# Optimization experiments

Measured on AMD Instinct MI355X. Metric: run time of the kernel, lower is better.

Reference implementation:

```python
import jax, jax.numpy as jnp
import numpy as np

B, NC, CARD, NCONT, DIM, DEPTH, HEADS, DH = 4096, 32, 100, 64, 64, 8, 8, 16
DEPTH = 6
INNER = HEADS * DH            # 128
TOTAL_TOKENS = NC * CARD + 2  # 3202 (2 special tokens)
CAT_FLAT = NC * DIM           # 2048
BETA = 0.2


def setup_inputs() -> dict:
    key = jax.random.key(0)
    ks = iter(jax.random.split(key, 32))
    n = lambda shape, s=0.05: jax.random.normal(next(ks), shape, dtype=jnp.float32) * s
    return {
        "x_categ": jax.random.randint(next(ks), (B, NC), 0, CARD),
        "x_cont": jax.random.normal(next(ks), (B, NCONT), dtype=jnp.float32),
        "embed": n((TOTAL_TOKENS, DIM)),
        "ln1_g": jnp.ones((DEPTH, DIM)), "ln1_b": jnp.zeros((DEPTH, DIM)),
        "wqkv": n((DEPTH, DIM, 3 * INNER)),
        "wo": n((DEPTH, INNER, DIM)), "bo": jnp.zeros((DEPTH, DIM)),
        "ln2_g": jnp.ones((DEPTH, DIM)), "ln2_b": jnp.zeros((DEPTH, DIM)),
        "wff1": n((DEPTH, DIM, 8 * DIM)), "bff1": jnp.zeros((DEPTH, 8 * DIM)),
        "wff2": n((DEPTH, 4 * DIM, DIM)), "bff2": jnp.zeros((DEPTH, DIM)),
        "bn_g": jnp.ones((NCONT,)), "bn_b": jnp.zeros((NCONT,)),
        "g0_w": n((CAT_FLAT + NCONT, CAT_FLAT)), "g0_b": jnp.zeros((CAT_FLAT,)),
        "h0_w": n((NCONT, CAT_FLAT)),
        "y1_w": n((CAT_FLAT, NCONT)), "y1_b": jnp.zeros((NCONT,)),
        "g1_w": n((2 * NCONT, NCONT)), "g1_b": jnp.zeros((NCONT,)),
        "h1_w": n((NCONT, NCONT)),
        "fc_w": n((CAT_FLAT + NCONT, 1)), "fc_b": jnp.zeros((1,)),
    }


def _ln(x, g, b):
    mu = x.mean(-1, keepdims=True)
    v = ((x - mu) ** 2).mean(-1, keepdims=True)
    return (x - mu) * jax.lax.rsqrt(v + 1e-5) * g + b


def _split_heads(t):  # [B, N, INNER] -> [B, H, N, DH]
    return t.reshape(B, NC, HEADS, DH).transpose(0, 2, 1, 3)


def _gate_combine(x, y, gw, gb, hw):
    # per-row gated aggregation with norm-scaled residual (DAG_combiner pair)
    g = jax.nn.relu(jnp.concatenate([x, y], axis=-1) @ gw + gb)
    H = g * (y @ hw)
    norm = jnp.linalg.norm(x, axis=1) / (jnp.linalg.norm(H, axis=1) + 1e-12)
    alpha = jnp.clip(norm * BETA, 0.0, 1.0)
    return x + alpha[:, None] * H


def reference(x_categ, x_cont, embed, ln1_g, ln1_b, wqkv, wo, bo, ln2_g, ln2_b,
              wff1, bff1, wff2, bff2, bn_g, bn_b, g0_w, g0_b, h0_w,
              y1_w, y1_b, g1_w, g1_b, h1_w, fc_w, fc_b):
    offsets = 2 + CARD * jnp.arange(NC)          # categories_offset
    tok = x_categ + offsets
    x = embed[tok]                                # [B, NC, DIM]
    scale = DH ** -0.5
    for d in range(DEPTH):
        h = _ln(x, ln1_g[d], ln1_b[d])
        q, k, v = jnp.split(h @ wqkv[d], 3, axis=-1)
        q, k, v = _split_heads(q), _split_heads(k), _split_heads(v)
        sim = jnp.einsum('bhid,bhjd->bhij', q, k) * scale
        attn = jax.nn.softmax(sim, axis=-1)
        o = jnp.einsum('bhij,bhjd->bhid', attn, v)
        o = o.transpose(0, 2, 1, 3).reshape(B, NC, INNER)
        x = x + (o @ wo[d] + bo[d])
        h = _ln(x, ln2_g[d], ln2_b[d])
        f = h @ wff1[d] + bff1[d]
        a, gg = jnp.split(f, 2, axis=-1)
        x = (a * jax.nn.gelu(gg, approximate=False)) @ wff2[d] + bff2[d] + x
    flat_categ = x.reshape(B, CAT_FLAT)
    # BatchNorm1d (train-mode batch stats, biased variance)
    mu = x_cont.mean(0)
    var = ((x_cont - mu) ** 2).mean(0)
    normed = (x_cont - mu) * jax.lax.rsqrt(var + 1e-5) * bn_g + bn_b
    # DAG combiner, dims = [2048, 64]
    c0 = _gate_combine(flat_categ, normed, g0_w, g0_b, h0_w)          # y_dim 64 <= 2048: no y proj
    y1 = flat_categ @ y1_w + y1_b                                      # y_dim 2048 > 64: MLP2 == single Linear
    c1 = _gate_combine(normed, y1, g1_w, g1_b, h1_w)
    logits = jnp.concatenate([c0, c1], axis=-1) @ fc_w + fc_b
    return jax.nn.sigmoid(logits)
```

## Files before the change

### kernel.cpp

```cpp
#include <hip/hip_runtime.h>
#include <hip/hip_bf16.h>

#define B_    4096
#define NC    32
#define DIM   64
#define INNER 128
#define HEADS 8
#define DH    16
#define DEPTH 6
#define NCONT 64
#define CATF  2048
#define KTOT  2112
#define NROW  (B_ * NC)

typedef __attribute__((ext_vector_type(8))) short short8;
typedef __attribute__((ext_vector_type(4))) float f32x4;
typedef __attribute__((ext_vector_type(16))) float f32x16;
typedef __attribute__((ext_vector_type(4))) unsigned short u16x4;

__device__ __forceinline__ float bf2f(__hip_bfloat16 h) { return __bfloat162float(h); }
__device__ __forceinline__ unsigned short f2bu(float f) {
    __hip_bfloat16 h = __float2bfloat16(f);
    return *(unsigned short*)&h;
}

__global__ __launch_bounds__(256) void k_wT(const float* __restrict__ W,
                                            __hip_bfloat16* __restrict__ WT,
                                            int K, int N)
{
    size_t idx = (size_t)blockIdx.x * 256 + threadIdx.x;
    int kn = K * N;
    int d = (int)(idx / kn), rem = (int)(idx % kn);
    int n = rem / K, k = rem % K;
    WT[idx] = __float2bfloat16(W[(size_t)d * kn + (size_t)k * N + n]);
}

__global__ __launch_bounds__(128) void k_former(
    const int* __restrict__ x_categ, const float* __restrict__ embed,
    const float* __restrict__ ln1_g, const float* __restrict__ ln1_b,
    const __hip_bfloat16* __restrict__ wqT, const __hip_bfloat16* __restrict__ woT,
    const float* __restrict__ bo,
    const float* __restrict__ ln2_g, const float* __restrict__ ln2_b,
    const __hip_bfloat16* __restrict__ w1T, const float* __restrict__ bff1,
    const __hip_bfloat16* __restrict__ w2T, const float* __restrict__ bff2,
    __hip_bfloat16* __restrict__ Acat)
{
    __shared__ __align__(16) unsigned char Ub[64 * 136 * 2];
    auto U  = reinterpret_cast<__hip_bfloat16(*)[136]>(Ub);
    auto Uf = reinterpret_cast<float(*)[68]>(Ub);
    __shared__ __align__(16) unsigned char QKb[2][3072];
    __shared__ __hip_bfloat16 vth[2][16][40];

    const int tid = threadIdx.x;
    const int w = tid >> 6, lane = tid & 63;
    const int lo = lane & 15, g = lane >> 4;
    const int q32 = lane & 31, hi = lane >> 5;
    const int r0 = blockIdx.x * 64;
    const f32x4 z4 = f32x4{0.f, 0.f, 0.f, 0.f};

    auto qhw = reinterpret_cast<__hip_bfloat16(*)[24]>(QKb[w]);
    auto khw = reinterpret_cast<__hip_bfloat16(*)[24]>(QKb[w] + 1536);
    auto psw = reinterpret_cast<__hip_bfloat16(*)[40]>(QKb[w]);

    float xacc[2][4][4];

    {
        int r = w * 32 + (lane >> 1), half = lane & 1;
        int grow = r0 + r;
        int tok = x_categ[grow] + 2 + 100 * (grow & 31);
        const float4* src = (const float4*)(embed + (size_t)tok * 64 + half * 32);
#pragma unroll
        for (int q4 = 0; q4 < 8; ++q4) {
            float4 v = src[q4];
            Uf[r][half * 32 + q4 * 4 + 0] = v.x; Uf[r][half * 32 + q4 * 4 + 1] = v.y;
            Uf[r][half * 32 + q4 * 4 + 2] = v.z; Uf[r][half * 32 + q4 * 4 + 3] = v.w;
        }
    }
#pragma unroll
    for (int mt = 0; mt < 2; ++mt)
#pragma unroll
        for (int nt = 0; nt < 4; ++nt)
#pragma unroll
            for (int rg = 0; rg < 4; ++rg)
                xacc[mt][nt][rg] = Uf[w * 32 + mt * 16 + g * 4 + rg][nt * 16 + lo];

    auto layernorm = [&](const float* gam, const float* bet) {
        float gv[4], bv_[4];
#pragma unroll
        for (int nt = 0; nt < 4; ++nt) { gv[nt] = gam[nt * 16 + lo]; bv_[nt] = bet[nt * 16 + lo]; }
#pragma unroll
        for (int mt = 0; mt < 2; ++mt)
#pragma unroll
            for (int rg = 0; rg < 4; ++rg) {
                float s = xacc[mt][0][rg] + xacc[mt][1][rg] + xacc[mt][2][rg] + xacc[mt][3][rg];
                float q = xacc[mt][0][rg] * xacc[mt][0][rg] + xacc[mt][1][rg] * xacc[mt][1][rg]
                        + xacc[mt][2][rg] * xacc[mt][2][rg] + xacc[mt][3][rg] * xacc[mt][3][rg];
#pragma unroll
                for (int m = 1; m < 16; m <<= 1) { s += __shfl_xor(s, m); q += __shfl_xor(q, m); }
                float mu = s * (1.f / 64.f);
                float var = q * (1.f / 64.f) - mu * mu;
                float ri = rsqrtf(var + 1e-5f);
                int token = w * 32 + mt * 16 + g * 4 + rg;
#pragma unroll
                for (int nt = 0; nt < 4; ++nt)
                    U[token][nt * 16 + lo] = __float2bfloat16((xacc[mt][nt][rg] - mu) * ri * gv[nt] + bv_[nt]);
            }
    };

#pragma unroll 1
    for (int d = 0; d < DEPTH; ++d) {
        const __hip_bfloat16* wq_d = wqT + (size_t)d * 384 * 64;
        const __hip_bfloat16* wo_d = woT + (size_t)d * 64 * 128;
        const __hip_bfloat16* w1_d = w1T + (size_t)d * 512 * 64;
        const __hip_bfloat16* w2_d = w2T + (size_t)d * 64 * 256;

        layernorm(ln1_g + d * 64, ln1_b + d * 64);

        short8 af[2][2];
#pragma unroll
        for (int mt = 0; mt < 2; ++mt)
#pragma unroll
            for (int kk = 0; kk < 2; ++kk)
                af[mt][kk] = *(const short8*)&U[w * 32 + mt * 16 + lo][kk * 32 + g * 8];

        for (int hh = 0; hh < HEADS; ++hh) {
            f32x4 aq[2] = {z4, z4}, ak[2] = {z4, z4}, av[2] = {z4, z4};
#pragma unroll
            for (int kk = 0; kk < 2; ++kk) {
                short8 bq  = *(const short8*)&wq_d[(size_t)(hh * 16 + lo) * 64 + kk * 32 + g * 8];
                short8 bk  = *(const short8*)&wq_d[(size_t)(128 + hh * 16 + lo) * 64 + kk * 32 + g * 8];
                short8 bv2 = *(const short8*)&wq_d[(size_t)(256 + hh * 16 + lo) * 64 + kk * 32 + g * 8];
#pragma unroll
                for (int mt = 0; mt < 2; ++mt) {
                    aq[mt] = __builtin_amdgcn_mfma_f32_16x16x32_bf16(af[mt][kk], bq,  aq[mt], 0, 0, 0);
                    ak[mt] = __builtin_amdgcn_mfma_f32_16x16x32_bf16(af[mt][kk], bk,  ak[mt], 0, 0, 0);
                    av[mt] = __builtin_amdgcn_mfma_f32_16x16x32_bf16(af[mt][kk], bv2, av[mt], 0, 0, 0);
                }
            }
#pragma unroll
            for (int mt = 0; mt < 2; ++mt) {
#pragma unroll
                for (int rg = 0; rg < 4; ++rg) {
                    int tok = mt * 16 + g * 4 + rg;
                    qhw[tok][lo] = __float2bfloat16(aq[mt][rg]);
                    khw[tok][lo] = __float2bfloat16(ak[mt][rg]);
                }
                u16x4 vv;
                vv.x = f2bu(av[mt][0]); vv.y = f2bu(av[mt][1]);
                vv.z = f2bu(av[mt][2]); vv.w = f2bu(av[mt][3]);
                *(u16x4*)&vth[w][lo][mt * 16 + g * 4] = vv;
            }
            short8 kaf = *(const short8*)&khw[q32][hi * 8];
            short8 qaf = *(const short8*)&qhw[q32][hi * 8];
            f32x16 z16{};
            f32x16 St = __builtin_amdgcn_mfma_f32_32x32x16_bf16(kaf, qaf, z16, 0, 0, 0);
            float sv[16];
            float mx = St[0] * 0.25f;
#pragma unroll
            for (int r = 0; r < 16; ++r) { sv[r] = St[r] * 0.25f; mx = fmaxf(mx, sv[r]); }
            mx = fmaxf(mx, __shfl_xor(mx, 32));
            float den = 0.f;
#pragma unroll
            for (int r = 0; r < 16; ++r) { sv[r] = __expf(sv[r] - mx); den += sv[r]; }
            den += __shfl_xor(den, 32);
            float rs = 1.f / den;
#pragma unroll
            for (int grp = 0; grp < 4; ++grp) {
                u16x4 pv;
                pv.x = f2bu(sv[grp * 4 + 0] * rs); pv.y = f2bu(sv[grp * 4 + 1] * rs);
                pv.z = f2bu(sv[grp * 4 + 2] * rs); pv.w = f2bu(sv[grp * 4 + 3] * rs);
                *(u16x4*)&psw[q32][grp * 8 + hi * 4] = pv;
            }
            short8 bv = *(const short8*)&vth[w][lo][g * 8];
#pragma unroll
            for (int qt = 0; qt < 2; ++qt) {
                int qrow = qt * 16 + lo;
                short8 ap = *(const short8*)&psw[qrow][g * 8];
                f32x4 ov = __builtin_amdgcn_mfma_f32_16x16x32_bf16(ap, bv, z4, 0, 0, 0);
#pragma unroll
                for (int rg = 0; rg < 4; ++rg)
                    U[w * 32 + qt * 16 + g * 4 + rg][hh * 16 + lo] = __float2bfloat16(ov[rg]);
            }
        }

        {
            short8 ap2[2][4];
#pragma unroll
            for (int mt = 0; mt < 2; ++mt)
#pragma unroll
                for (int kk = 0; kk < 4; ++kk)
                    ap2[mt][kk] = *(const short8*)&U[w * 32 + mt * 16 + lo][kk * 32 + g * 8];
            f32x4 pacc[2][4];
#pragma unroll
            for (int mt = 0; mt < 2; ++mt)
#pragma unroll
                for (int nt = 0; nt < 4; ++nt) pacc[mt][nt] = z4;
#pragma unroll
            for (int kk = 0; kk < 4; ++kk)
#pragma unroll
                for (int nt = 0; nt < 4; ++nt) {
                    short8 b = *(const short8*)&wo_d[(size_t)(nt * 16 + lo) * 128 + kk * 32 + g * 8];
#pragma unroll
                    for (int mt = 0; mt < 2; ++mt)
                        pacc[mt][nt] = __builtin_amdgcn_mfma_f32_16x16x32_bf16(ap2[mt][kk], b, pacc[mt][nt], 0, 0, 0);
                }
            float bov[4];
#pragma unroll
            for (int nt = 0; nt < 4; ++nt) bov[nt] = bo[d * 64 + nt * 16 + lo];
#pragma unroll
            for (int mt = 0; mt < 2; ++mt)
#pragma unroll
                for (int nt = 0; nt < 4; ++nt)
#pragma unroll
                    for (int rg = 0; rg < 4; ++rg)
                        xacc[mt][nt][rg] += pacc[mt][nt][rg] + bov[nt];
        }

        layernorm(ln2_g + d * 64, ln2_b + d * 64);

        {
            short8 af2[2][2];
#pragma unroll
            for (int mt = 0; mt < 2; ++mt)
#pragma unroll
                for (int kk = 0; kk < 2; ++kk)
                    af2[mt][kk] = *(const short8*)&U[w * 32 + mt * 16 + lo][kk * 32 + g * 8];
            f32x4 acc2[2][4];
#pragma unroll
            for (int mt = 0; mt < 2; ++mt)
#pragma unroll
                for (int nt = 0; nt < 4; ++nt) acc2[mt][nt] = z4;

            for (int c4 = 0; c4 < 4; ++c4) {
#pragma unroll
                for (int nh = 0; nh < 2; ++nh) {
                    f32x4 aa[2][2], agg[2][2];
#pragma unroll
                    for (int mt = 0; mt < 2; ++mt)
#pragma unroll
                        for (int nj = 0; nj < 2; ++nj) { aa[mt][nj] = z4; agg[mt][nj] = z4; }
#pragma unroll
                    for (int kk = 0; kk < 2; ++kk)
#pragma unroll
                        for (int nj = 0; nj < 2; ++nj) {
                            int nt = nh * 2 + nj;
                            short8 ba = *(const short8*)&w1_d[(size_t)(c4 * 64 + nt * 16 + lo) * 64 + kk * 32 + g * 8];
                            short8 bg = *(const short8*)&w1_d[(size_t)(256 + c4 * 64 + nt * 16 + lo) * 64 + kk * 32 + g * 8];
#pragma unroll
                            for (int mt = 0; mt < 2; ++mt) {
                                aa[mt][nj]  = __builtin_amdgcn_mfma_f32_16x16x32_bf16(af2[mt][kk], ba, aa[mt][nj], 0, 0, 0);
                                agg[mt][nj] = __builtin_amdgcn_mfma_f32_16x16x32_bf16(af2[mt][kk], bg, agg[mt][nj], 0, 0, 0);
                            }
                        }
#pragma unroll
                    for (int mt = 0; mt < 2; ++mt)
#pragma unroll
                        for (int nj = 0; nj < 2; ++nj)
#pragma unroll
                            for (int rg = 0; rg < 4; ++rg) {
                                int nt = nh * 2 + nj;
                                int col = c4 * 64 + nt * 16 + lo;
                                float a  = aa[mt][nj][rg]  + bff1[d * 512 + col];
                                float gg = agg[mt][nj][rg] + bff1[d * 512 + 256 + col];
                                float g2 = gg * gg;
                                float t  = gg * (1.f + 0.044715f * g2);
                                float e  = __expf(1.5957691216f * t);
                                float gl = gg * e * __builtin_amdgcn_rcpf(e + 1.f);
                                U[w * 32 + mt * 16 + g * 4 + rg][nt * 16 + lo] = __float2bfloat16(a * gl);
                            }
                }
                short8 apg[2][2];
#pragma unroll
                for (int mt = 0; mt < 2; ++mt)
#pragma unroll
                    for (int kk = 0; kk < 2; ++kk)
                        apg[mt][kk] = *(const short8*)&U[w * 32 + mt * 16 + lo][kk * 32 + g * 8];
#pragma unroll
                for (int kk = 0; kk < 2; ++kk)
#pragma unroll
                    for (int nt = 0; nt < 4; ++nt) {
                        short8 bb = *(const short8*)&w2_d[(size_t)(nt * 16 + lo) * 256 + c4 * 64 + kk * 32 + g * 8];
#pragma unroll
                        for (int mt = 0; mt < 2; ++mt)
                            acc2[mt][nt] = __builtin_amdgcn_mfma_f32_16x16x32_bf16(apg[mt][kk], bb, acc2[mt][nt], 0, 0, 0);
                    }
            }
            float b2v[4];
#pragma unroll
            for (int nt = 0; nt < 4; ++nt) b2v[nt] = bff2[d * 64 + nt * 16 + lo];
#pragma unroll
            for (int mt = 0; mt < 2; ++mt)
#pragma unroll
                for (int nt = 0; nt < 4; ++nt)
#pragma unroll
                    for (int rg = 0; rg < 4; ++rg)
                        xacc[mt][nt][rg] += acc2[mt][nt][rg] + b2v[nt];
        }
    }

    {
        size_t base = (size_t)(blockIdx.x * 2 + w) * KTOT;
#pragma unroll
        for (int mt = 0; mt < 2; ++mt)
#pragma unroll
            for (int rg = 0; rg < 4; ++rg) {
                int token = mt * 16 + g * 4 + rg;
#pragma unroll
                for (int nt = 0; nt < 4; ++nt)
                    Acat[base + token * 64 + nt * 16 + lo] = __float2bfloat16(xacc[mt][nt][rg]);
            }
    }
}

__global__ __launch_bounds__(256) void k_bn(
    const float* __restrict__ x_cont, const float* __restrict__ bn_g, const float* __restrict__ bn_b,
    float* __restrict__ normed, __hip_bfloat16* __restrict__ Acat)
{
    const int c = blockIdx.x;
    const int tid = threadIdx.x;
    float sum = 0.f, sq = 0.f;
    for (int rr = tid; rr < B_; rr += 256) { float v = x_cont[rr * NCONT + c]; sum += v; sq += v * v; }
    __shared__ float ssum[256], ssq[256];
    ssum[tid] = sum; ssq[tid] = sq;
    __syncthreads();
    for (int st = 128; st > 0; st >>= 1) {
        if (tid < st) { ssum[tid] += ssum[tid + st]; ssq[tid] += ssq[tid + st]; }
        __syncthreads();
    }
    float mu  = ssum[0] * (1.f / B_);
    float var = ssq[0] * (1.f / B_) - mu * mu;
    float ri  = rsqrtf(var + 1e-5f);
    float gg = bn_g[c], bb = bn_b[c];
    for (int rr = tid; rr < B_; rr += 256) {
        float v = (x_cont[rr * NCONT + c] - mu) * ri * gg + bb;
        normed[rr * NCONT + c] = v;
        Acat[(size_t)rr * KTOT + CATF + c] = __float2bfloat16(v);
    }
}

__global__ __launch_bounds__(256) void k_transpose(
    const float* __restrict__ W, __hip_bfloat16* __restrict__ WT)
{
    __shared__ float tile[64][65];
    const int n0 = blockIdx.x * 64, k0 = blockIdx.y * 64;
    const int tid = threadIdx.x;
    for (int e = tid; e < 64 * 16; e += 256) {
        int rr = e >> 4, c4 = e & 15;
        float4 v = *(const float4*)&W[(size_t)(k0 + rr) * CATF + n0 + c4 * 4];
        tile[rr][c4 * 4 + 0] = v.x; tile[rr][c4 * 4 + 1] = v.y;
        tile[rr][c4 * 4 + 2] = v.z; tile[rr][c4 * 4 + 3] = v.w;
    }
    __syncthreads();
    for (int e = tid; e < 64 * 32; e += 256) {
        int n = e >> 5, kp = e & 31;
        __hip_bfloat16 h0 = __float2bfloat16(tile[kp * 2 + 0][n]);
        __hip_bfloat16 h1 = __float2bfloat16(tile[kp * 2 + 1][n]);
        unsigned u = ((unsigned)(*(unsigned short*)&h1) << 16) | (unsigned)(*(unsigned short*)&h0);
        *(unsigned*)&WT[(size_t)(n0 + n) * KTOT + k0 + kp * 2] = u;
    }
}

__global__ __launch_bounds__(256) void k_gemm_g0(
    const __hip_bfloat16* __restrict__ Acat, const __hip_bfloat16* __restrict__ WT,
    const float* __restrict__ g0_b, __hip_bfloat16* __restrict__ G)
{
    __shared__ __hip_bfloat16 At[128][72];
    __shared__ __hip_bfloat16 Bt[128][72];
    const int tid = threadIdx.x;
    const int m0 = blockIdx.y * 128, n0 = blockIdx.x * 128;
    const int w = tid >> 6, lane = tid & 63, g = lane >> 4;
    const int wr = w >> 1, wc = w & 1;

    f32x4 acc[4][4];
#pragma unroll
    for (int mi = 0; mi < 4; ++mi)
#pragma unroll
        for (int ni = 0; ni < 4; ++ni) acc[mi][ni] = f32x4{0.f, 0.f, 0.f, 0.f};

    const int row_a = wr * 64 + (lane & 15);
    const int row_b = wc * 64 + (lane & 15);

    for (int kt = 0; kt < KTOT / 64; ++kt) {
        const int k0 = kt * 64;
#pragma unroll
        for (int t = 0; t < 4; ++t) {
            int e = tid + t * 256; int rr = e >> 3, seg = e & 7;
            *(uint4*)&At[rr][seg * 8] = *(const uint4*)&Acat[(size_t)(m0 + rr) * KTOT + k0 + seg * 8];
        }
#pragma unroll
        for (int t = 0; t < 4; ++t) {
            int e = tid + t * 256; int rr = e >> 3, seg = e & 7;
            *(uint4*)&Bt[rr][seg * 8] = *(const uint4*)&WT[(size_t)(n0 + rr) * KTOT + k0 + seg * 8];
        }
        __syncthreads();
        short8 af[4][2], bfr[4][2];
#pragma unroll
        for (int mi = 0; mi < 4; ++mi)
#pragma unroll
            for (int kk = 0; kk < 2; ++kk)
                af[mi][kk] = *(const short8*)&At[row_a + mi * 16][kk * 32 + g * 8];
#pragma unroll
        for (int ni = 0; ni < 4; ++ni)
#pragma unroll
            for (int kk = 0; kk < 2; ++kk)
                bfr[ni][kk] = *(const short8*)&Bt[row_b + ni * 16][kk * 32 + g * 8];
#pragma unroll
        for (int kk = 0; kk < 2; ++kk)
#pragma unroll
            for (int mi = 0; mi < 4; ++mi)
#pragma unroll
                for (int ni = 0; ni < 4; ++ni)
                    acc[mi][ni] = __builtin_amdgcn_mfma_f32_16x16x32_bf16(af[mi][kk], bfr[ni][kk], acc[mi][ni], 0, 0, 0);
        __syncthreads();
    }

#pragma unroll
    for (int mi = 0; mi < 4; ++mi)
#pragma unroll
        for (int ni = 0; ni < 4; ++ni)
#pragma unroll
            for (int reg = 0; reg < 4; ++reg) {
                int row = m0 + wr * 64 + mi * 16 + (lane >> 4) * 4 + reg;
                int col = n0 + wc * 64 + ni * 16 + (lane & 15);
                float v = acc[mi][ni][reg] + g0_b[col];
                G[(size_t)row * CATF + col] = __float2bfloat16(fmaxf(v, 0.f));
            }
}

__global__ __launch_bounds__(256) void k_y1v2(
    const __hip_bfloat16* __restrict__ Acat, const __hip_bfloat16* __restrict__ y1T,
    const float* __restrict__ y1_b, float* __restrict__ y1)
{
    __shared__ __hip_bfloat16 At[128][136];
    __shared__ __hip_bfloat16 Bt[64][136];
    const int tid = threadIdx.x;
    const size_t m0 = (size_t)blockIdx.x * 128;
    const int w = tid >> 6, lane = tid & 63, lo = lane & 15, g = lane >> 4;
    f32x4 acc[2][4];
#pragma unroll
    for (int mt = 0; mt < 2; ++mt)
#pragma unroll
        for (int nt = 0; nt < 4; ++nt) acc[mt][nt] = f32x4{0.f, 0.f, 0.f, 0.f};
    for (int kt = 0; kt < 16; ++kt) {
        if (kt) __syncthreads();
#pragma unroll
        for (int t = 0; t < 8; ++t) {
            int e = tid + t * 256; int row = e >> 4, seg = e & 15;
            *(uint4*)&At[row][seg * 8] = *(const uint4*)&Acat[(m0 + row) * KTOT + kt * 128 + seg * 8];
        }
#pragma unroll
        for (int t = 0; t < 4; ++t) {
            int e = tid + t * 256; int row = e >> 4, seg = e & 15;
            *(uint4*)&Bt[row][seg * 8] = *(const uint4*)&y1T[(size_t)row * 2048 + kt * 128 + seg * 8];
        }
        __syncthreads();
#pragma unroll
        for (int kk = 0; kk < 4; ++kk) {
            short8 a[2], b[4];
#pragma unroll
            for (int mt = 0; mt < 2; ++mt) a[mt] = *(const short8*)&At[w * 32 + mt * 16 + lo][kk * 32 + g * 8];
#pragma unroll
            for (int nt = 0; nt < 4; ++nt) b[nt] = *(const short8*)&Bt[nt * 16 + lo][kk * 32 + g * 8];
#pragma unroll
            for (int mt = 0; mt < 2; ++mt)
#pragma unroll
                for (int nt = 0; nt < 4; ++nt)
                    acc[mt][nt] = __builtin_amdgcn_mfma_f32_16x16x32_bf16(a[mt], b[nt], acc[mt][nt], 0, 0, 0);
        }
    }
#pragma unroll
    for (int mt = 0; mt < 2; ++mt)
#pragma unroll
        for (int nt = 0; nt < 4; ++nt)
#pragma unroll
            for (int rg = 0; rg < 4; ++rg) {
                size_t row = m0 + w * 32 + mt * 16 + g * 4 + rg;
                int col = nt * 16 + lo;
                y1[row * 64 + col] = acc[mt][nt][rg] + y1_b[col];
            }
}

__global__ __launch_bounds__(256) void k_H2(
    const __hip_bfloat16* __restrict__ Acat, const __hip_bfloat16* __restrict__ h0T,
    __hip_bfloat16* __restrict__ G)
{
    __shared__ __hip_bfloat16 At[128][72];
    const int tid = threadIdx.x;
    const int m0 = blockIdx.y * 128, n0 = blockIdx.x * 128;
    const int w = tid >> 6, lane = tid & 63, lo = lane & 15, g = lane >> 4;
    const int wr = w >> 1, wc = w & 1;
#pragma unroll
    for (int t = 0; t < 4; ++t) {
        int e = tid + t * 256; int row = e >> 3, seg = e & 7;
        *(uint4*)&At[row][seg * 8] = *(const uint4*)&Acat[(size_t)(m0 + row) * KTOT + CATF + seg * 8];
    }
    __syncthreads();
    f32x4 acc[4][4];
#pragma unroll
    for (int mt = 0; mt < 4; ++mt)
#pragma unroll
        for (int nt = 0; nt < 4; ++nt) acc[mt][nt] = f32x4{0.f, 0.f, 0.f, 0.f};
#pragma unroll
    for (int kk = 0; kk < 2; ++kk) {
        short8 a[4], b[4];
#pragma unroll
        for (int mt = 0; mt < 4; ++mt) a[mt] = *(const short8*)&At[wr * 64 + mt * 16 + lo][kk * 32 + g * 8];
#pragma unroll
        for (int nt = 0; nt < 4; ++nt)
            b[nt] = *(const short8*)&h0T[(size_t)(n0 + wc * 64 + nt * 16 + lo) * 64 + kk * 32 + g * 8];
#pragma unroll
        for (int mt = 0; mt < 4; ++mt)
#pragma unroll
            for (int nt = 0; nt < 4; ++nt)
                acc[mt][nt] = __builtin_amdgcn_mfma_f32_16x16x32_bf16(a[mt], b[nt], acc[mt][nt], 0, 0, 0);
    }
#pragma unroll
    for (int mt = 0; mt < 4; ++mt)
#pragma unroll
        for (int nt = 0; nt < 4; ++nt)
#pragma unroll
            for (int rg = 0; rg < 4; ++rg) {
                size_t row = (size_t)m0 + wr * 64 + mt * 16 + g * 4 + rg;
                int col = n0 + wc * 64 + nt * 16 + lo;
                size_t offo = row * CATF + col;
                G[offo] = __float2bfloat16(bf2f(G[offo]) * acc[mt][nt][rg]);
            }
}

__global__ __launch_bounds__(256) void k_final(
    const __hip_bfloat16* __restrict__ Acat, const __hip_bfloat16* __restrict__ H,
    const float* __restrict__ normed, const float* __restrict__ y1,
    const float* __restrict__ g1_w, const float* __restrict__ g1_b, const float* __restrict__ h1_w,
    const float* __restrict__ fc_w, const float* __restrict__ fc_b,
    float* __restrict__ out)
{
    const int b = blockIdx.x;
    const int tid = threadIdx.x;
    const __hip_bfloat16* xrow = Acat + (size_t)b * KTOT;
    const __hip_bfloat16* hrow = H + (size_t)b * CATF;

    __shared__ float r1[256], r2[256];
    float sx = 0.f, sh = 0.f;
    for (int n = tid; n < CATF; n += 256) {
        float xv = bf2f(xrow[n]); sx += xv * xv;
        float hv = bf2f(hrow[n]); sh += hv * hv;
    }
    r1[tid] = sx; r2[tid] = sh;
    __syncthreads();
    for (int st = 128; st > 0; st >>= 1) {
        if (tid < st) { r1[tid] += r1[tid + st]; r2[tid] += r2[tid + st]; }
        __syncthreads();
    }
    float alpha0 = fminf(fmaxf(sqrtf(r1[0]) / (sqrtf(r2[0]) + 1e-12f) * 0.2f, 0.f), 1.f);
    __syncthreads();

    float pd = 0.f;
    for (int n = tid; n < CATF; n += 256) {
        float c0 = bf2f(xrow[n]) + alpha0 * bf2f(hrow[n]);
        pd += c0 * fc_w[n];
    }
    r1[tid] = pd;
    __syncthreads();
    for (int st = 128; st > 0; st >>= 1) {
        if (tid < st) r1[tid] += r1[tid + st];
        __syncthreads();
    }
    float dot0 = r1[0];

    __shared__ float ny[128];
    __shared__ float c1dot;
    if (tid < 64) ny[tid] = normed[b * NCONT + tid];
    else if (tid < 128) ny[tid] = y1[b * NCONT + tid - 64];
    __syncthreads();

    if (tid < 64) {
        const int j = tid;
        float g = g1_b[j];
        for (int k = 0; k < 128; ++k) g += ny[k] * g1_w[k * 64 + j];
        g = fmaxf(g, 0.f);
        float hv = 0.f;
        for (int k = 0; k < 64; ++k) hv += ny[64 + k] * h1_w[k * 64 + j];
        float H1 = g * hv;
        float nj = ny[j];
        float snx = nj * nj, snh = H1 * H1;
        for (int m = 1; m < 64; m <<= 1) { snx += __shfl_xor(snx, m, 64); snh += __shfl_xor(snh, m, 64); }
        float a1 = fminf(fmaxf(sqrtf(snx) / (sqrtf(snh) + 1e-12f) * 0.2f, 0.f), 1.f);
        float d1 = (nj + a1 * H1) * fc_w[CATF + j];
        for (int m = 1; m < 64; m <<= 1) d1 += __shfl_xor(d1, m, 64);
        if (tid == 0) c1dot = d1;
    }
    __syncthreads();
    if (tid == 0) {
        float logit = dot0 + c1dot + fc_b[0];
        out[b] = 1.f / (1.f + expf(-logit));
    }
}

extern "C" void kernel_launch(void* const* d_in, const int* in_sizes, int n_in,
                              void* d_out, int out_size, void* d_ws, size_t ws_size,
                              hipStream_t stream)
{
    const int*   x_categ = (const int*)d_in[0];
    const float* x_cont  = (const float*)d_in[1];
    const float* embed   = (const float*)d_in[2];
    const float* ln1_g   = (const float*)d_in[3];
    const float* ln1_b   = (const float*)d_in[4];
    const float* wqkv    = (const float*)d_in[5];
    const float* wo      = (const float*)d_in[6];
    const float* bo      = (const float*)d_in[7];
    const float* ln2_g   = (const float*)d_in[8];
    const float* ln2_b   = (const float*)d_in[9];
    const float* wff1    = (const float*)d_in[10];
    const float* bff1    = (const float*)d_in[11];
    const float* wff2    = (const float*)d_in[12];
    const float* bff2    = (const float*)d_in[13];
    const float* bn_g    = (const float*)d_in[14];
    const float* bn_b    = (const float*)d_in[15];
    const float* g0_w    = (const float*)d_in[16];
    const float* g0_b    = (const float*)d_in[17];
    const float* h0_w    = (const float*)d_in[18];
    const float* y1_w    = (const float*)d_in[19];
    const float* y1_b    = (const float*)d_in[20];
    const float* g1_w    = (const float*)d_in[21];
    const float* g1_b    = (const float*)d_in[22];
    const float* h1_w    = (const float*)d_in[23];
    const float* fc_w    = (const float*)d_in[24];
    const float* fc_b    = (const float*)d_in[25];

    char* ws = (char*)d_ws;
    size_t off = 0;
    auto alloc = [&](size_t bytes) { void* pp = ws + off; off += (bytes + 255) & ~255ULL; return pp; };
    __hip_bfloat16* wqT  = (__hip_bfloat16*)alloc((size_t)DEPTH * 384 * 64 * 2);
    __hip_bfloat16* woT  = (__hip_bfloat16*)alloc((size_t)DEPTH * 64 * 128 * 2);
    __hip_bfloat16* w1T  = (__hip_bfloat16*)alloc((size_t)DEPTH * 512 * 64 * 2);
    __hip_bfloat16* w2T  = (__hip_bfloat16*)alloc((size_t)DEPTH * 64 * 256 * 2);
    __hip_bfloat16* h0T  = (__hip_bfloat16*)alloc((size_t)CATF * 64 * 2);
    __hip_bfloat16* y1T  = (__hip_bfloat16*)alloc((size_t)CATF * 64 * 2);
    __hip_bfloat16* Acat = (__hip_bfloat16*)alloc((size_t)B_ * KTOT * 2);
    __hip_bfloat16* WT   = (__hip_bfloat16*)alloc((size_t)CATF * KTOT * 2);
    __hip_bfloat16* G    = (__hip_bfloat16*)alloc((size_t)B_ * CATF * 2);
    float*          norm = (float*)alloc((size_t)B_ * NCONT * 4);
    float*          y1v  = (float*)alloc((size_t)B_ * NCONT * 4);

    k_wT<<<576, 256, 0, stream>>>(wqkv, wqT, 64, 384);
    k_wT<<<192, 256, 0, stream>>>(wo,   woT, 128, 64);
    k_wT<<<768, 256, 0, stream>>>(wff1, w1T, 64, 512);
    k_wT<<<384, 256, 0, stream>>>(wff2, w2T, 256, 64);
    k_wT<<<512, 256, 0, stream>>>(h0_w, h0T, 64, 2048);
    k_wT<<<512, 256, 0, stream>>>(y1_w, y1T, 2048, 64);

    k_former<<<NROW / 64, 128, 0, stream>>>(x_categ, embed, ln1_g, ln1_b, wqT, woT, bo,
                                            ln2_g, ln2_b, w1T, bff1, w2T, bff2, Acat);

    k_bn<<<NCONT, 256, 0, stream>>>(x_cont, bn_g, bn_b, norm, Acat);
    k_transpose<<<dim3(CATF / 64, KTOT / 64), 256, 0, stream>>>(g0_w, WT);
    k_gemm_g0<<<dim3(CATF / 128, B_ / 128), 256, 0, stream>>>(Acat, WT, g0_b, G);
    k_y1v2<<<B_ / 128, 256, 0, stream>>>(Acat, y1T, y1_b, y1v);
    k_H2<<<dim3(CATF / 128, B_ / 128), 256, 0, stream>>>(Acat, h0T, G);
    k_final<<<B_, 256, 0, stream>>>(Acat, G, norm, y1v, g1_w, g1_b, h1_w, fc_w, fc_b, (float*)d_out);
}
```

Measured before the change: 745.9 us.

## Interleave out-projection with head groups to shrink shared-memory tile

Splits the eight attention heads into two groups of four and accumulates the output projection after each group, so the per-warp attention output buffer only needs 64 columns. The shared tile shrinks from 64x136 to 64x72 bf16, and the embedding gather now loads straight into registers instead of staging through shared memory as fp32. The aim is lower LDS use per block, allowing more resident blocks per CU, plus one fewer staging pass. The projection accumulators stay live across the head loop, which raises register pressure and could cost occupancy back.

Result: slower. 1.105 ms (+48.2%).

```diff
diff --git a/kernel.cpp b/kernel.cpp
--- a/kernel.cpp
+++ b/kernel.cpp
@@ -45,9 +45,7 @@
     const __hip_bfloat16* __restrict__ w2T, const float* __restrict__ bff2,
     __hip_bfloat16* __restrict__ Acat)
 {
-    __shared__ __align__(16) unsigned char Ub[64 * 136 * 2];
-    auto U  = reinterpret_cast<__hip_bfloat16(*)[136]>(Ub);
-    auto Uf = reinterpret_cast<float(*)[68]>(Ub);
+    __shared__ __align__(16) __hip_bfloat16 U[64][72];
     __shared__ __align__(16) unsigned char QKb[2][3072];
     __shared__ __hip_bfloat16 vth[2][16][40];
 
@@ -64,25 +62,18 @@
 
     float xacc[2][4][4];
 
-    {
-        int r = w * 32 + (lane >> 1), half = lane & 1;
-        int grow = r0 + r;
-        int tok = x_categ[grow] + 2 + 100 * (grow & 31);
-        const float4* src = (const float4*)(embed + (size_t)tok * 64 + half * 32);
-#pragma unroll
-        for (int q4 = 0; q4 < 8; ++q4) {
-            float4 v = src[q4];
-            Uf[r][half * 32 + q4 * 4 + 0] = v.x; Uf[r][half * 32 + q4 * 4 + 1] = v.y;
-            Uf[r][half * 32 + q4 * 4 + 2] = v.z; Uf[r][half * 32 + q4 * 4 + 3] = v.w;
-        }
-    }
 #pragma unroll
     for (int mt = 0; mt < 2; ++mt)
 #pragma unroll
-        for (int nt = 0; nt < 4; ++nt)
-#pragma unroll
-            for (int rg = 0; rg < 4; ++rg)
-                xacc[mt][nt][rg] = Uf[w * 32 + mt * 16 + g * 4 + rg][nt * 16 + lo];
+        for (int rg = 0; rg < 4; ++rg) {
+            int r = w * 32 + mt * 16 + g * 4 + rg;
+            int grow = r0 + r;
+            int tok = x_categ[grow] + 2 + 100 * (grow & 31);
+            const float* erow = embed + (size_t)tok * 64 + lo;
+#pragma unroll
+            for (int nt = 0; nt < 4; ++nt)
+                xacc[mt][nt][rg] = erow[nt * 16];
+        }
 
     auto layernorm = [&](const float* gam, const float* bet) {
         float gv[4], bv_[4];
@@ -123,87 +114,88 @@
             for (int kk = 0; kk < 2; ++kk)
                 af[mt][kk] = *(const short8*)&U[w * 32 + mt * 16 + lo][kk * 32 + g * 8];
 
-        for (int hh = 0; hh < HEADS; ++hh) {
-            f32x4 aq[2] = {z4, z4}, ak[2] = {z4, z4}, av[2] = {z4, z4};
-#pragma unroll
-            for (int kk = 0; kk < 2; ++kk) {
-                short8 bq  = *(const short8*)&wq_d[(size_t)(hh * 16 + lo) * 64 + kk * 32 + g * 8];
-                short8 bk  = *(const short8*)&wq_d[(size_t)(128 + hh * 16 + lo) * 64 + kk * 32 + g * 8];
-                short8 bv2 = *(const short8*)&wq_d[(size_t)(256 + hh * 16 + lo) * 64 + kk * 32 + g * 8];
+        f32x4 pacc[2][4];
+#pragma unroll
+        for (int mt = 0; mt < 2; ++mt)
+#pragma unroll
+            for (int nt = 0; nt < 4; ++nt) pacc[mt][nt] = z4;
+
+#pragma unroll 1
+        for (int hg = 0; hg < 2; ++hg) {
+            for (int h4 = 0; h4 < 4; ++h4) {
+                const int hh = hg * 4 + h4;
+                f32x4 aq[2] = {z4, z4}, ak[2] = {z4, z4}, av[2] = {z4, z4};
+#pragma unroll
+                for (int kk = 0; kk < 2; ++kk) {
+                    short8 bq  = *(const short8*)&wq_d[(size_t)(hh * 16 + lo) * 64 + kk * 32 + g * 8];
+                    short8 bk  = *(const short8*)&wq_d[(size_t)(128 + hh * 16 + lo) * 64 + kk * 32 + g * 8];
+                    short8 bv2 = *(const short8*)&wq_d[(size_t)(256 + hh * 16 + lo) * 64 + kk * 32 + g * 8];
+#pragma unroll
+                    for (int mt = 0; mt < 2; ++mt) {
+                        aq[mt] = __builtin_amdgcn_mfma_f32_16x16x32_bf16(af[mt][kk], bq,  aq[mt], 0, 0, 0);
+                        ak[mt] = __builtin_amdgcn_mfma_f32_16x16x32_bf16(af[mt][kk], bk,  ak[mt], 0, 0, 0);
+                        av[mt] = __builtin_amdgcn_mfma_f32_16x16x32_bf16(af[mt][kk], bv2, av[mt], 0, 0, 0);
+                    }
+                }
 #pragma unroll
                 for (int mt = 0; mt < 2; ++mt) {
-                    aq[mt] = __builtin_amdgcn_mfma_f32_16x16x32_bf16(af[mt][kk], bq,  aq[mt], 0, 0, 0);
-                    ak[mt] = __builtin_amdgcn_mfma_f32_16x16x32_bf16(af[mt][kk], bk,  ak[mt], 0, 0, 0);
-                    av[mt] = __builtin_amdgcn_mfma_f32_16x16x32_bf16(af[mt][kk], bv2, av[mt], 0, 0, 0);
+#pragma unroll
+                    for (int rg = 0; rg < 4; ++rg) {
+                        int tok = mt * 16 + g * 4 + rg;
+                        qhw[tok][lo] = __float2bfloat16(aq[mt][rg]);
+                        khw[tok][lo] = __float2bfloat16(ak[mt][rg]);
+                    }
+                    u16x4 vv;
+                    vv.x = f2bu(av[mt][0]); vv.y = f2bu(av[mt][1]);
+                    vv.z = f2bu(av[mt][2]); vv.w = f2bu(av[mt][3]);
+                    *(u16x4*)&vth[w][lo][mt * 16 + g * 4] = vv;
                 }
-            }
-#pragma unroll
-            for (int mt = 0; mt < 2; ++mt) {
-#pragma unroll
-                for (int rg = 0; rg < 4; ++rg) {
-                    int tok = mt * 16 + g * 4 + rg;
-                    qhw[tok][lo] = __float2bfloat16(aq[mt][rg]);
-                    khw[tok][lo] = __float2bfloat16(ak[mt][rg]);
+                short8 kaf = *(const short8*)&khw[q32][hi * 8];
+                short8 qaf = *(const short8*)&qhw[q32][hi * 8];
+                f32x16 z16{};
+                f32x16 St = __builtin_amdgcn_mfma_f32_32x32x16_bf16(kaf, qaf, z16, 0, 0, 0);
+                float sv[16];
+                float mx = St[0] * 0.25f;
+#pragma unroll
+                for (int r = 0; r < 16; ++r) { sv[r] = St[r] * 0.25f; mx = fmaxf(mx, sv[r]); }
+                mx = fmaxf(mx, __shfl_xor(mx, 32));
+                float den = 0.f;
+#pragma unroll
+                for (int r = 0; r < 16; ++r) { sv[r] = __expf(sv[r] - mx); den += sv[r]; }
+                den += __shfl_xor(den, 32);
+                float rs = 1.f / den;
+#pragma unroll
+                for (int grp = 0; grp < 4; ++grp) {
+                    u16x4 pv;
+                    pv.x = f2bu(sv[grp * 4 + 0] * rs); pv.y = f2bu(sv[grp * 4 + 1] * rs);
+                    pv.z = f2bu(sv[grp * 4 + 2] * rs); pv.w = f2bu(sv[grp * 4 + 3] * rs);
+                    *(u16x4*)&psw[q32][grp * 8 + hi * 4] = pv;
                 }
-                u16x4 vv;
-                vv.x = f2bu(av[mt][0]); vv.y = f2bu(av[mt][1]);
-                vv.z = f2bu(av[mt][2]); vv.w = f2bu(av[mt][3]);
-                *(u16x4*)&vth[w][lo][mt * 16 + g * 4] = vv;
-            }
-            short8 kaf = *(const short8*)&khw[q32][hi * 8];
-            short8 qaf = *(const short8*)&qhw[q32][hi * 8];
-            f32x16 z16{};
-            f32x16 St = __builtin_amdgcn_mfma_f32_32x32x16_bf16(kaf, qaf, z16, 0, 0, 0);
-            float sv[16];
-            float mx = St[0] * 0.25f;
-#pragma unroll
-            for (int r = 0; r < 16; ++r) { sv[r] = St[r] * 0.25f; mx = fmaxf(mx, sv[r]); }
-            mx = fmaxf(mx, __shfl_xor(mx, 32));
-            float den = 0.f;
-#pragma unroll
-            for (int r = 0; r < 16; ++r) { sv[r] = __expf(sv[r] - mx); den += sv[r]; }
-            den += __shfl_xor(den, 32);
-            float rs = 1.f / den;
-#pragma unroll
-            for (int grp = 0; grp < 4; ++grp) {
-                u16x4 pv;
-                pv.x = f2bu(sv[grp * 4 + 0] * rs); pv.y = f2bu(sv[grp * 4 + 1] * rs);
-                pv.z = f2bu(sv[grp * 4 + 2] * rs); pv.w = f2bu(sv[grp * 4 + 3] * rs);
-                *(u16x4*)&psw[q32][grp * 8 + hi * 4] = pv;
-            }
-            short8 bv = *(const short8*)&vth[w][lo][g * 8];
-#pragma unroll
-            for (int qt = 0; qt < 2; ++qt) {
-                int qrow = qt * 16 + lo;
-                short8 ap = *(const short8*)&psw[qrow][g * 8];
-                f32x4 ov = __builtin_amdgcn_mfma_f32_16x16x32_bf16(ap, bv, z4, 0, 0, 0);
-#pragma unroll
-                for (int rg = 0; rg < 4; ++rg)
-                    U[w * 32 + qt * 16 + g * 4 + rg][hh * 16 + lo] = __float2bfloat16(ov[rg]);
+                short8 bv = *(const short8*)&vth[w][lo][g * 8];
+#pragma unroll
+                for (int qt = 0; qt < 2; ++qt) {
+                    int qrow = qt * 16 + lo;
+                    short8 ap = *(const short8*)&psw[qrow][g * 8];
+                    f32x4 ov = __builtin_amdgcn_mfma_f32_16x16x32_bf16(ap, bv, z4, 0, 0, 0);
+#pragma unroll
+                    for (int rg = 0; rg < 4; ++rg)
+                        U[w * 32 + qt * 16 + g * 4 + rg][h4 * 16 + lo] = __float2bfloat16(ov[rg]);
+                }
+            }
+#pragma unroll
+            for (int kl = 0; kl < 2; ++kl) {
+                short8 a0 = *(const short8*)&U[w * 32 + lo][kl * 32 + g * 8];
+                short8 a1 = *(const short8*)&U[w * 32 + 16 + lo][kl * 32 + g * 8];
+#pragma unroll
+                for (int nt = 0; nt < 4; ++nt) {
+                    short8 b = *(const short8*)&wo_d[(size_t)(nt * 16 + lo) * 128 + (hg * 2 + kl) * 32 + g * 8];
+                    pacc[0][nt] = __builtin_amdgcn_mfma_f32_16x16x32_bf16(a0, b, pacc[0][nt], 0, 0, 0);
+                    pacc[1][nt] = __builtin_amdgcn_mfma_f32_16x16x32_bf16(a1, b, pacc[1][nt], 0, 0, 0);
+                }
             }
         }
 
         {
-            short8 ap2[2][4];
-#pragma unroll
-            for (int mt = 0; mt < 2; ++mt)
-#pragma unroll
-                for (int kk = 0; kk < 4; ++kk)
-                    ap2[mt][kk] = *(const short8*)&U[w * 32 + mt * 16 + lo][kk * 32 + g * 8];
-            f32x4 pacc[2][4];
-#pragma unroll
-            for (int mt = 0; mt < 2; ++mt)
-#pragma unroll
-                for (int nt = 0; nt < 4; ++nt) pacc[mt][nt] = z4;
-#pragma unroll
-            for (int kk = 0; kk < 4; ++kk)
-#pragma unroll
-                for (int nt = 0; nt < 4; ++nt) {
-                    short8 b = *(const short8*)&wo_d[(size_t)(nt * 16 + lo) * 128 + kk * 32 + g * 8];
-#pragma unroll
-                    for (int mt = 0; mt < 2; ++mt)
-                        pacc[mt][nt] = __builtin_amdgcn_mfma_f32_16x16x32_bf16(ap2[mt][kk], b, pacc[mt][nt], 0, 0, 0);
-                }
             float bov[4];
 #pragma unroll
             for (int nt = 0; nt < 4; ++nt) bov[nt] = bo[d * 64 + nt * 16 + lo];
```
